# Kernel tuning notes

Hardware: AMD Instinct MI355X
Metric: run time of the kernel (lower is better)

Reference implementation:

```python
import jax, jax.numpy as jnp
import numpy as np

G, P, F, K = 256, 512, 4, 6   # graphs, nodes/graph, features, knn k
N = G * P

def _prelu(x, a):
    return jnp.where(x >= 0, x, a * x)

def _knn_edges(x):
    # per-graph brute-force kNN (k=6, no self loops), flow source->target
    xg = x.reshape(G, P, F)
    sq = jnp.sum(xg * xg, -1)                                   # [G,P]
    d = sq[:, :, None] + sq[:, None, :] - 2.0 * jnp.einsum('gpf,gqf->gpq', xg, xg)
    d = d + jnp.eye(P, dtype=x.dtype) * 1e10                    # exclude self
    _, idx = jax.lax.top_k(-d, K)                               # [G,P,K] neighbors
    off = (jnp.arange(G) * P)[:, None, None]
    src = (idx + off).reshape(-1)                               # message sources
    tgt = jnp.broadcast_to(jnp.arange(N).reshape(G, P, 1), (G, P, K)).reshape(-1)
    return src, tgt

def setup_inputs():
    key = jax.random.key(0)
    ks = jax.random.split(key, 8)
    f = lambda k, s: jax.random.normal(k, s, jnp.float32) * 0.1
    return {
        "x": jax.random.normal(ks[0], (N, F), jnp.float32),
        "batch": jnp.arange(N, dtype=jnp.int32) // P,
        "pre_W1": f(ks[1], (F, F)), "pre_b1": jnp.zeros((F,), jnp.float32),
        "pre_a1": jnp.full((F,), 0.25, jnp.float32),
        "pre_W2": f(ks[2], (F, F)), "pre_b2": jnp.zeros((F,), jnp.float32),
        "pre_a2": jnp.full((F,), 0.25, jnp.float32),
        "bn_g": jnp.ones((F,), jnp.float32), "bn_b": jnp.zeros((F,), jnp.float32),
        "act_a": jnp.full((F,), 0.25, jnp.float32),
        "conv_Wm": f(ks[3], (4, F, F)), "conv_bm": jnp.zeros((4, F), jnp.float32),
        "hlv_W1": f(ks[4], (5 * F, 5 * F)), "hlv_b1": jnp.zeros((5 * F,), jnp.float32),
        "hlv_W2": f(ks[5], (5 * F, 1)), "hlv_b2": jnp.zeros((1,), jnp.float32),
    }

def reference(x, batch, pre_W1, pre_b1, pre_a1, pre_W2, pre_b2, pre_a2,
              bn_g, bn_b, act_a, conv_Wm, conv_bm, hlv_W1, hlv_b1, hlv_W2, hlv_b2):
    src, tgt = _knn_edges(x)                                    # knn on raw x
    # pre_nn: Linear-PReLU-Linear-PReLU-BatchNorm (batch stats, training mode)
    h = _prelu(x @ pre_W1 + pre_b1, pre_a1)
    h = _prelu(h @ pre_W2 + pre_b2, pre_a2)
    mu = jnp.mean(h, 0)
    var = jnp.var(h, 0)
    h = (h - mu) / jnp.sqrt(var + 1e-5) * bn_g + bn_b
    xs = [h]
    for i in range(4):
        # GeneralConv (PyG defaults): sum-aggregate lin_msg(x_j) + identity skip
        msg = h[src] @ conv_Wm[i] + conv_bm[i]                  # [E,F]
        aggr = jax.ops.segment_sum(msg, tgt, num_segments=N)    # [N,F]
        h = _prelu(aggr + h, act_a)                             # shared PReLU act
        xs.append(h)
    hc = jnp.concatenate(xs, axis=-1)                           # JK 'cat' -> [N,5F]
    pooled = jax.ops.segment_sum(hc, batch, num_segments=G)     # global_add_pool
    out = jax.nn.relu(pooled @ hlv_W1 + hlv_b1) @ hlv_W2 + hlv_b2
    return out
```

## Files before the change

### kernel.cpp

```cpp
#include <hip/hip_runtime.h>

#define GG 256
#define PP 512
#define FF 4
#define KK 6
#define NN (GG*PP)

__device__ __forceinline__ unsigned umin_(unsigned a, unsigned b){ return a<b?a:b; }
__device__ __forceinline__ unsigned umax_(unsigned a, unsigned b){ return a>b?a:b; }
__device__ __forceinline__ float finf(){ return __int_as_float(0x7f800000); }

__device__ __forceinline__ unsigned mmap32(float d){
    int bb = __float_as_int(d);
    int t = bb >> 31;
    return (unsigned)(bb ^ (t | (int)0x80000000));
}

__device__ __forceinline__ void cas6_u64(uint64_t (&B)[6], uint64_t kv)
{
    bool c1 = kv < B[1]; bool c2 = kv < B[2]; bool c3 = kv < B[3];
    bool c4 = kv < B[4]; bool c5 = kv < B[5];
    B[0] = c1 ? B[1] : kv;
    B[1] = c2 ? B[2] : (c1 ? kv : B[1]);
    B[2] = c3 ? B[3] : (c2 ? kv : B[2]);
    B[3] = c4 ? B[4] : (c3 ? kv : B[3]);
    B[4] = c5 ? B[5] : (c4 ? kv : B[4]);
    B[5] = c5 ? kv : B[5];
}

#define INS7U(v){                                  \
    unsigned n0=umin_(M0,(v));                     \
    unsigned n1=umin_(M1,umax_((v),M0));           \
    unsigned n2=umin_(M2,umax_((v),M1));           \
    unsigned n3=umin_(M3,umax_((v),M2));           \
    unsigned n4=umin_(M4,umax_((v),M3));           \
    unsigned n5=umin_(M5,umax_((v),M4));           \
    unsigned n6=umin_(M6,umax_((v),M5));           \
    M0=n0;M1=n1;M2=n2;M3=n3;M4=n4;M5=n5;M6=n6; }

__global__ __launch_bounds__(512, 4) void scan_kernel(
    const float* __restrict__ x,
    const float* __restrict__ pre_W1, const float* __restrict__ pre_b1, const float* __restrict__ pre_a1,
    const float* __restrict__ pre_W2, const float* __restrict__ pre_b2, const float* __restrict__ pre_a2,
    float* __restrict__ bn_part,
    int* __restrict__ knn_idx)
{
    __shared__ float4   xm2s[PP];
    __shared__ float    sqs[PP];
    __shared__ unsigned ubuf[16*256];
    __shared__ float    Tv[256];
    __shared__ float    wred[8][8];

    ushort   (*gmp16)[256] = (ushort  (*)[256])ubuf;
    unsigned (*mbuf)[256]  = (unsigned(*)[256])ubuf;

    const int t = threadIdx.x;
    const int bid = blockIdx.x;
    const int g = bid >> 1, half = bid & 1;
    const int tbase = half * 256;
    const int gbase = g * PP;
    const int w = t >> 6, lane = t & 63;
    const int wu = __builtin_amdgcn_readfirstlane(w);
    const int qb = wu * 64;

    float4 xt = ((const float4*)x)[gbase + t];
    xm2s[t] = make_float4(-2.0f*xt.x, -2.0f*xt.y, -2.0f*xt.z, -2.0f*xt.w);
    sqs[t]  = xt.x*xt.x + xt.y*xt.y + xt.z*xt.z + xt.w*xt.w;
    if (half == 0){
        float h1[FF], h2[FF];
#pragma unroll
        for (int fo=0;fo<FF;fo++){
            float m = xt.x*pre_W1[0*FF+fo] + xt.y*pre_W1[1*FF+fo]
                    + xt.z*pre_W1[2*FF+fo] + xt.w*pre_W1[3*FF+fo] + pre_b1[fo];
            h1[fo] = m >= 0.0f ? m : pre_a1[fo]*m;
        }
#pragma unroll
        for (int fo=0;fo<FF;fo++){
            float m = h1[0]*pre_W2[0*FF+fo] + h1[1]*pre_W2[1*FF+fo]
                    + h1[2]*pre_W2[2*FF+fo] + h1[3]*pre_W2[3*FF+fo] + pre_b2[fo];
            h2[fo] = m >= 0.0f ? m : pre_a2[fo]*m;
        }
        float v[8];
#pragma unroll
        for (int f=0;f<4;f++){ v[f]=h2[f]; v[4+f]=h2[f]*h2[f]; }
#pragma unroll
        for (int off=32; off; off>>=1){
#pragma unroll
            for (int f=0;f<8;f++) v[f] += __shfl_down(v[f], off);
        }
        if (lane==0){
#pragma unroll
            for (int f=0;f<8;f++) wred[w][f]=v[f];
        }
    }
    __syncthreads();
    if (half == 0 && t < 8){
        float a=0;
#pragma unroll
        for (int w2=0;w2<8;w2++) a += wred[w2][t];
        bn_part[t*GG + g] = a;
    }

    float4 xp[4];
#pragma unroll
    for (int j=0;j<4;j++){
        float4 v = xm2s[tbase + lane + 64*j];
        xp[j] = make_float4(-0.5f*v.x, -0.5f*v.y, -0.5f*v.z, -0.5f*v.w);
    }
    const float INF = finf();

#pragma unroll 1
    for (int grp=0; grp<4; grp++){
        float gm[4];
#pragma unroll
        for (int j=0;j<4;j++) gm[j]=INF;
#pragma unroll
        for (int i2=0;i2<8;i2++){
            const int q0 = qb + grp*16 + i2*2;
            float4 a = xm2s[q0], b = xm2s[q0+1];
            float2 sq = *(const float2*)&sqs[q0];
#pragma unroll
            for (int j=0;j<4;j++){
                float da = fmaf(a.x,xp[j].x, fmaf(a.y,xp[j].y, fmaf(a.z,xp[j].z, fmaf(a.w,xp[j].w, sq.x))));
                float db = fmaf(b.x,xp[j].x, fmaf(b.y,xp[j].y, fmaf(b.z,xp[j].z, fmaf(b.w,xp[j].w, sq.y))));
                gm[j] = fminf(gm[j], fminf(da, db));
            }
        }
#pragma unroll
        for (int j=0;j<4;j++){
            unsigned u = mmap32(gm[j]);
            unsigned r = (u >> 16) + ((u & 0xFFFFu) ? 1u : 0u);
            r = umin_(r, 0xFFFFu);
            gmp16[wu*4 + grp][lane + 64*j] = (ushort)r;
        }
    }
    __syncthreads();

    if (t < 256){
        unsigned M0=~0u,M1=~0u,M2=~0u,M3=~0u,M4=~0u,M5=~0u,M6=~0u;
#pragma unroll
        for (int r=0;r<32;r++){
            unsigned v = gmp16[r][t];
            INS7U(v);
        }
        unsigned Tc = M6 << 16;
        Tv[t] = (Tc & 0x80000000u) ? __uint_as_float(Tc ^ 0x80000000u)
                                   : __uint_as_float(~Tc);
    }
    __syncthreads();

    float Tf[4];
#pragma unroll
    for (int j=0;j<4;j++) Tf[j] = Tv[lane + 64*j];

#pragma unroll 1
    for (int h=0; h<2; h++){
        unsigned m[4];
#pragma unroll
        for (int j=0;j<4;j++) m[j]=0;
#pragma unroll 4
        for (int i2=0;i2<16;i2++){
            const int q0 = qb + h*32 + i2*2;
            float4 a = xm2s[q0], b = xm2s[q0+1];
            float2 sq = *(const float2*)&sqs[q0];
#pragma unroll
            for (int j=0;j<4;j++){
                float da = fmaf(a.x,xp[j].x, fmaf(a.y,xp[j].y, fmaf(a.z,xp[j].z, fmaf(a.w,xp[j].w, sq.x))));
                float db = fmaf(b.x,xp[j].x, fmaf(b.y,xp[j].y, fmaf(b.z,xp[j].z, fmaf(b.w,xp[j].w, sq.y))));
                m[j] = m[j] + m[j] + (da <= Tf[j] ? 1u : 0u);
                m[j] = m[j] + m[j] + (db <= Tf[j] ? 1u : 0u);
            }
        }
#pragma unroll
        for (int j=0;j<4;j++) mbuf[wu*2 + h][lane + 64*j] = m[j];
    }
    __syncthreads();

    if (t < 256){
        const int pt = tbase + t;
        float4 xmq = xm2s[pt];
        float4 xq = make_float4(-0.5f*xmq.x, -0.5f*xmq.y, -0.5f*xmq.z, -0.5f*xmq.w);
        uint64_t B[6];
#pragma unroll
        for (int j2=0;j2<6;j2++) B[j2] = ~0ull;
#pragma unroll 1
        for (int r=0;r<16;r++){
            unsigned m = mbuf[r][t];
            const int base = (r>>1)*64 + (r&1)*32;
            while (m){
                int c = __builtin_clz(m);
                m &= ~(0x80000000u >> c);
                int idx = base + c;
                float4 a = xm2s[idx];
                float d = fmaf(a.x,xq.x, fmaf(a.y,xq.y, fmaf(a.z,xq.z, fmaf(a.w,xq.w, sqs[idx]))));
                uint64_t key = ((uint64_t)mmap32(d) << 32) | (unsigned)idx;
                if (idx == pt) key = ~0ull;
                if (key < B[0]) cas6_u64(B, key);
            }
        }
#pragma unroll
        for (int j2=0;j2<6;j2++)
            knn_idx[j2*NN + gbase + pt] = (int)(B[j2] & 0xFFFFFFFFull);
    }
}

__global__ __launch_bounds__(512) void graph_kernel(
    const float* __restrict__ x,
    const int* __restrict__ knn_idx,
    const float* __restrict__ bn_part,
    const float* __restrict__ pre_W1, const float* __restrict__ pre_b1, const float* __restrict__ pre_a1,
    const float* __restrict__ pre_W2, const float* __restrict__ pre_b2, const float* __restrict__ pre_a2,
    const float* __restrict__ bn_g, const float* __restrict__ bn_b,
    const float* __restrict__ act_a,
    const float* __restrict__ conv_Wm, const float* __restrict__ conv_bm,
    const float* __restrict__ hlv_W1, const float* __restrict__ hlv_b1,
    const float* __restrict__ hlv_W2, const float* __restrict__ hlv_b2,
    float* __restrict__ out)
{
    __shared__ float4 hbuf[PP];
    __shared__ float wred[8][4];
    __shared__ float pooled[20];
    __shared__ float stats[8];
    __shared__ float hid[20];
    const int g = blockIdx.x, p = threadIdx.x;
    const int gp = g*PP + p;

    if (p < 64){
        int vv = p>>3, j = p&7;
        float acc = 0.0f;
        for (int i=j;i<GG;i+=8) acc += bn_part[vv*GG + i];
        acc += __shfl_xor(acc,1); acc += __shfl_xor(acc,2); acc += __shfl_xor(acc,4);
        if (j==0) stats[vv] = acc;
    }
    __syncthreads();
    if (p < 4){
        float mu  = stats[p]   * (1.0f/NN);
        float var = stats[4+p] * (1.0f/NN) - mu*mu;
        stats[p]   = mu;
        stats[4+p] = 1.0f / sqrtf(var + 1e-5f);
    }

    float4 xt = ((const float4*)x)[gp];
    float h1[FF], h2[FF];
#pragma unroll
    for (int fo=0;fo<FF;fo++){
        float m = xt.x*pre_W1[0*FF+fo] + xt.y*pre_W1[1*FF+fo]
                + xt.z*pre_W1[2*FF+fo] + xt.w*pre_W1[3*FF+fo] + pre_b1[fo];
        h1[fo] = m >= 0.0f ? m : pre_a1[fo]*m;
    }
#pragma unroll
    for (int fo=0;fo<FF;fo++){
        float m = h1[0]*pre_W2[0*FF+fo] + h1[1]*pre_W2[1*FF+fo]
                + h1[2]*pre_W2[2*FF+fo] + h1[3]*pre_W2[3*FF+fo] + pre_b2[fo];
        h2[fo] = m >= 0.0f ? m : pre_a2[fo]*m;
    }
    __syncthreads();

    float hp[4];
#pragma unroll
    for (int f=0;f<4;f++)
        hp[f] = (h2[f] - stats[f]) * stats[4+f] * bn_g[f] + bn_b[f];
    hbuf[p] = make_float4(hp[0],hp[1],hp[2],hp[3]);
    int nb[KK];
#pragma unroll
    for (int j=0;j<KK;j++) nb[j] = knn_idx[j*NN + gp];

    auto block_accum = [&](const float* h, int slice){
        float v0=h[0], v1=h[1], v2=h[2], v3=h[3];
#pragma unroll
        for (int off=32; off; off>>=1){
            v0 += __shfl_down(v0,off); v1 += __shfl_down(v1,off);
            v2 += __shfl_down(v2,off); v3 += __shfl_down(v3,off);
        }
        int w = p>>6;
        if ((p&63)==0){ wred[w][0]=v0; wred[w][1]=v1; wred[w][2]=v2; wred[w][3]=v3; }
        __syncthreads();
        if (p < 4){
            float a=0;
#pragma unroll
            for (int w2=0;w2<8;w2++) a += wred[w2][p];
            pooled[slice*4+p] = a;
        }
        __syncthreads();
    };

    block_accum(hp, 0);

#pragma unroll 1
    for (int L=0; L<4; L++){
        float4 sm = make_float4(0.f,0.f,0.f,0.f);
#pragma unroll
        for (int j=0;j<KK;j++){
            float4 hn = hbuf[nb[j]];
            sm.x+=hn.x; sm.y+=hn.y; sm.z+=hn.z; sm.w+=hn.w;
        }
        const float* W  = conv_Wm + L*16;
        const float* bm = conv_bm + L*4;
        float nh[4];
#pragma unroll
        for (int fo=0;fo<4;fo++){
            float m = sm.x*W[0*4+fo] + sm.y*W[1*4+fo] + sm.z*W[2*4+fo] + sm.w*W[3*4+fo]
                    + 6.0f*bm[fo] + hp[fo];
            float a = act_a[fo];
            nh[fo] = m >= 0.0f ? m : a*m;
        }
        __syncthreads();
        hbuf[p] = make_float4(nh[0],nh[1],nh[2],nh[3]);
#pragma unroll
        for (int f=0;f<4;f++) hp[f]=nh[f];
        block_accum(hp, L+1);
    }

    if (p < 20){
        float acc = hlv_b1[p];
#pragma unroll 1
        for (int k2=0;k2<20;k2++) acc += pooled[k2]*hlv_W1[k2*20+p];
        hid[p] = acc > 0.0f ? acc : 0.0f;
    }
    __syncthreads();
    if (p == 0){
        float o = hlv_b2[0];
#pragma unroll 1
        for (int j=0;j<20;j++) o += hid[j]*hlv_W2[j];
        out[g] = o;
    }
}

extern "C" void kernel_launch(void* const* d_in, const int* in_sizes, int n_in,
                              void* d_out, int out_size, void* d_ws, size_t ws_size,
                              hipStream_t stream)
{
    const float* x      = (const float*)d_in[0];
    const float* pre_W1 = (const float*)d_in[2];
    const float* pre_b1 = (const float*)d_in[3];
    const float* pre_a1 = (const float*)d_in[4];
    const float* pre_W2 = (const float*)d_in[5];
    const float* pre_b2 = (const float*)d_in[6];
    const float* pre_a2 = (const float*)d_in[7];
    const float* bn_g   = (const float*)d_in[8];
    const float* bn_b   = (const float*)d_in[9];
    const float* act_a  = (const float*)d_in[10];
    const float* conv_Wm= (const float*)d_in[11];
    const float* conv_bm= (const float*)d_in[12];
    const float* hlv_W1 = (const float*)d_in[13];
    const float* hlv_b1 = (const float*)d_in[14];
    const float* hlv_W2 = (const float*)d_in[15];
    const float* hlv_b2 = (const float*)d_in[16];

    char* ws = (char*)d_ws;
    int*   knn     = (int*)ws;
    float* bn_part = (float*)(ws + (size_t)6*NN*sizeof(int));

    scan_kernel<<<GG*2, PP, 0, stream>>>(x, pre_W1,pre_b1,pre_a1,
                                         pre_W2,pre_b2,pre_a2, bn_part, knn);
    graph_kernel<<<GG, PP, 0, stream>>>(x, knn, bn_part,
                                        pre_W1,pre_b1,pre_a1, pre_W2,pre_b2,pre_a2,
                                        bn_g,bn_b, act_a, conv_Wm,conv_bm,
                                        hlv_W1,hlv_b1,hlv_W2,hlv_b2,
                                        (float*)d_out);
}
```

Before: 58.80 us.

## Split kNN scan into quarter-graph blocks and replace bitmask pass with group-pruned exact scan

```diff
diff --git a/kernel.cpp b/kernel.cpp
--- a/kernel.cpp
+++ b/kernel.cpp
@@ -38,7 +38,7 @@
     unsigned n6=umin_(M6,umax_((v),M5));           \
     M0=n0;M1=n1;M2=n2;M3=n3;M4=n4;M5=n5;M6=n6; }
 
-__global__ __launch_bounds__(512, 4) void scan_kernel(
+__global__ __launch_bounds__(512, 8) void scan_kernel(
     const float* __restrict__ x,
     const float* __restrict__ pre_W1, const float* __restrict__ pre_b1, const float* __restrict__ pre_a1,
     const float* __restrict__ pre_W2, const float* __restrict__ pre_b2, const float* __restrict__ pre_a2,
@@ -47,17 +47,14 @@
 {
     __shared__ float4   xm2s[PP];
     __shared__ float    sqs[PP];
-    __shared__ unsigned ubuf[16*256];
-    __shared__ float    Tv[256];
+    __shared__ ushort   gmp16[32][128];
+    __shared__ uint64_t pairbuf[128][6];
     __shared__ float    wred[8][8];
-
-    ushort   (*gmp16)[256] = (ushort  (*)[256])ubuf;
-    unsigned (*mbuf)[256]  = (unsigned(*)[256])ubuf;
 
     const int t = threadIdx.x;
     const int bid = blockIdx.x;
-    const int g = bid >> 1, half = bid & 1;
-    const int tbase = half * 256;
+    const int g = bid >> 2, quarter = bid & 3;
+    const int tbase = quarter * 128;
     const int gbase = g * PP;
     const int w = t >> 6, lane = t & 63;
     const int wu = __builtin_amdgcn_readfirstlane(w);
@@ -66,7 +63,7 @@
     float4 xt = ((const float4*)x)[gbase + t];
     xm2s[t] = make_float4(-2.0f*xt.x, -2.0f*xt.y, -2.0f*xt.z, -2.0f*xt.w);
     sqs[t]  = xt.x*xt.x + xt.y*xt.y + xt.z*xt.z + xt.w*xt.w;
-    if (half == 0){
+    if (quarter == 0){
         float h1[FF], h2[FF];
 #pragma unroll
         for (int fo=0;fo<FF;fo++){
@@ -94,16 +91,16 @@
         }
     }
     __syncthreads();
-    if (half == 0 && t < 8){
+    if (quarter == 0 && t < 8){
         float a=0;
 #pragma unroll
         for (int w2=0;w2<8;w2++) a += wred[w2][t];
         bn_part[t*GG + g] = a;
     }
 
-    float4 xp[4];
-#pragma unroll
-    for (int j=0;j<4;j++){
+    float4 xp[2];
+#pragma unroll
+    for (int j=0;j<2;j++){
         float4 v = xm2s[tbase + lane + 64*j];
         xp[j] = make_float4(-0.5f*v.x, -0.5f*v.y, -0.5f*v.z, -0.5f*v.w);
     }
@@ -111,23 +108,25 @@
 
 #pragma unroll 1
     for (int grp=0; grp<4; grp++){
-        float gm[4];
-#pragma unroll
-        for (int j=0;j<4;j++) gm[j]=INF;
-#pragma unroll
-        for (int i2=0;i2<8;i2++){
-            const int q0 = qb + grp*16 + i2*2;
-            float4 a = xm2s[q0], b = xm2s[q0+1];
-            float2 sq = *(const float2*)&sqs[q0];
-#pragma unroll
-            for (int j=0;j<4;j++){
-                float da = fmaf(a.x,xp[j].x, fmaf(a.y,xp[j].y, fmaf(a.z,xp[j].z, fmaf(a.w,xp[j].w, sq.x))));
-                float db = fmaf(b.x,xp[j].x, fmaf(b.y,xp[j].y, fmaf(b.z,xp[j].z, fmaf(b.w,xp[j].w, sq.y))));
-                gm[j] = fminf(gm[j], fminf(da, db));
+        float gm[2];
+        gm[0]=INF; gm[1]=INF;
+#pragma unroll
+        for (int i4=0;i4<4;i4++){
+            const int q0 = qb + grp*16 + i4*4;
+            float4 a0 = xm2s[q0],   a1 = xm2s[q0+1];
+            float4 a2 = xm2s[q0+2], a3 = xm2s[q0+3];
+            float4 sq = *(const float4*)&sqs[q0];
+#pragma unroll
+            for (int j=0;j<2;j++){
+                float d0 = fmaf(a0.x,xp[j].x, fmaf(a0.y,xp[j].y, fmaf(a0.z,xp[j].z, fmaf(a0.w,xp[j].w, sq.x))));
+                float d1 = fmaf(a1.x,xp[j].x, fmaf(a1.y,xp[j].y, fmaf(a1.z,xp[j].z, fmaf(a1.w,xp[j].w, sq.y))));
+                float d2 = fmaf(a2.x,xp[j].x, fmaf(a2.y,xp[j].y, fmaf(a2.z,xp[j].z, fmaf(a2.w,xp[j].w, sq.z))));
+                float d3 = fmaf(a3.x,xp[j].x, fmaf(a3.y,xp[j].y, fmaf(a3.z,xp[j].z, fmaf(a3.w,xp[j].w, sq.w))));
+                gm[j] = fminf(gm[j], fminf(fminf(d0,d1), fminf(d2,d3)));
             }
         }
 #pragma unroll
-        for (int j=0;j<4;j++){
+        for (int j=0;j<2;j++){
             unsigned u = mmap32(gm[j]);
             unsigned r = (u >> 16) + ((u & 0xFFFFu) ? 1u : 0u);
             r = umin_(r, 0xFFFFu);
@@ -136,71 +135,52 @@
     }
     __syncthreads();
 
+    uint64_t B[6];
+#pragma unroll
+    for (int j2=0;j2<6;j2++) B[j2] = ~0ull;
     if (t < 256){
+        const int tgt = t >> 1, m = t & 1;
+        const int pt = tbase + tgt;
         unsigned M0=~0u,M1=~0u,M2=~0u,M3=~0u,M4=~0u,M5=~0u,M6=~0u;
 #pragma unroll
         for (int r=0;r<32;r++){
-            unsigned v = gmp16[r][t];
+            unsigned v = gmp16[r][tgt];
             INS7U(v);
         }
-        unsigned Tc = M6 << 16;
-        Tv[t] = (Tc & 0x80000000u) ? __uint_as_float(Tc ^ 0x80000000u)
-                                   : __uint_as_float(~Tc);
-    }
-    __syncthreads();
-
-    float Tf[4];
-#pragma unroll
-    for (int j=0;j<4;j++) Tf[j] = Tv[lane + 64*j];
-
-#pragma unroll 1
-    for (int h=0; h<2; h++){
-        unsigned m[4];
-#pragma unroll
-        for (int j=0;j<4;j++) m[j]=0;
-#pragma unroll 4
-        for (int i2=0;i2<16;i2++){
-            const int q0 = qb + h*32 + i2*2;
-            float4 a = xm2s[q0], b = xm2s[q0+1];
-            float2 sq = *(const float2*)&sqs[q0];
-#pragma unroll
-            for (int j=0;j<4;j++){
-                float da = fmaf(a.x,xp[j].x, fmaf(a.y,xp[j].y, fmaf(a.z,xp[j].z, fmaf(a.w,xp[j].w, sq.x))));
-                float db = fmaf(b.x,xp[j].x, fmaf(b.y,xp[j].y, fmaf(b.z,xp[j].z, fmaf(b.w,xp[j].w, sq.y))));
-                m[j] = m[j] + m[j] + (da <= Tf[j] ? 1u : 0u);
-                m[j] = m[j] + m[j] + (db <= Tf[j] ? 1u : 0u);
-            }
-        }
-#pragma unroll
-        for (int j=0;j<4;j++) mbuf[wu*2 + h][lane + 64*j] = m[j];
-    }
-    __syncthreads();
-
-    if (t < 256){
-        const int pt = tbase + t;
+        const unsigned Tc = M6;
         float4 xmq = xm2s[pt];
         float4 xq = make_float4(-0.5f*xmq.x, -0.5f*xmq.y, -0.5f*xmq.z, -0.5f*xmq.w);
-        uint64_t B[6];
-#pragma unroll
-        for (int j2=0;j2<6;j2++) B[j2] = ~0ull;
-#pragma unroll 1
-        for (int r=0;r<16;r++){
-            unsigned m = mbuf[r][t];
-            const int base = (r>>1)*64 + (r&1)*32;
-            while (m){
-                int c = __builtin_clz(m);
-                m &= ~(0x80000000u >> c);
-                int idx = base + c;
-                float4 a = xm2s[idx];
-                float d = fmaf(a.x,xq.x, fmaf(a.y,xq.y, fmaf(a.z,xq.z, fmaf(a.w,xq.w, sqs[idx]))));
-                uint64_t key = ((uint64_t)mmap32(d) << 32) | (unsigned)idx;
-                if (idx == pt) key = ~0ull;
-                if (key < B[0]) cas6_u64(B, key);
+#pragma unroll 1
+        for (int r=m; r<32; r+=2){
+            if ((unsigned)gmp16[r][tgt] <= Tc){
+                const int base = r*16;
+#pragma unroll 4
+                for (int c=0;c<16;c++){
+                    const int idx = base + c;
+                    float4 a = xm2s[idx];
+                    float d = fmaf(a.x,xq.x, fmaf(a.y,xq.y, fmaf(a.z,xq.z, fmaf(a.w,xq.w, sqs[idx]))));
+                    uint64_t key = ((uint64_t)mmap32(d) << 32) | (unsigned)idx;
+                    if (idx == pt) key = ~0ull;
+                    if (key < B[0]) cas6_u64(B, key);
+                }
             }
         }
+        if (m == 1){
+#pragma unroll
+            for (int j2=0;j2<6;j2++) pairbuf[tgt][j2] = B[j2];
+        }
+    }
+    __syncthreads();
+    if (t < 256 && (t & 1) == 0){
+        const int tgt = t >> 1;
+#pragma unroll
+        for (int j2=0;j2<6;j2++){
+            uint64_t key = pairbuf[tgt][j2];
+            if (key < B[0]) cas6_u64(B, key);
+        }
 #pragma unroll
         for (int j2=0;j2<6;j2++)
-            knn_idx[j2*NN + gbase + pt] = (int)(B[j2] & 0xFFFFFFFFull);
+            knn_idx[j2*NN + gbase + tbase + tgt] = (int)(B[j2] & 0xFFFFFFFFull);
     }
 }
 
@@ -351,7 +331,7 @@
     int*   knn     = (int*)ws;
     float* bn_part = (float*)(ws + (size_t)6*NN*sizeof(int));
 
-    scan_kernel<<<GG*2, PP, 0, stream>>>(x, pre_W1,pre_b1,pre_a1,
+    scan_kernel<<<GG*4, PP, 0, stream>>>(x, pre_W1,pre_b1,pre_a1,
                                          pre_W2,pre_b2,pre_a2, bn_part, knn);
     graph_kernel<<<GG, PP, 0, stream>>>(x, knn, bn_part,
                                         pre_W1,pre_b1,pre_a1, pre_W2,pre_b2,pre_a2,
```

Result: slower. 166.6 us (+183.3%).
